# Kernel tuning notes

Hardware: AMD Instinct MI355X
Metric: run time of the kernel (lower is better)

## Reference

```python
import jax, jax.numpy as jnp
import numpy as np

B, D, O, A, H, NL = 1024, 512, 8, 64, 1024, 2

def setup_inputs() -> dict:
    key = jax.random.key(0)
    ks = jax.random.split(key, 8)
    s = 0.02
    return {
        "state": jax.random.normal(ks[0], (B, D), jnp.float32),
        # option network: Linear(D,H) -> ReLU -> Linear(H,O)
        "ow1": jax.random.normal(ks[1], (D, H), jnp.float32) * s, "ob1": jnp.zeros((H,), jnp.float32),
        "ow2": jax.random.normal(ks[2], (H, O), jnp.float32) * s, "ob2": jnp.zeros((O,), jnp.float32),
        # stacked action networks (one per option): Linear(D,H) -> act -> [Linear(H,H) -> act]*(NL-1) -> Linear(H,A)
        "aw1": jax.random.normal(ks[3], (O, D, H), jnp.float32) * s, "ab1": jnp.zeros((O, H), jnp.float32),
        "awh": jax.random.normal(ks[4], (O, NL - 1, H, H), jnp.float32) * s, "abh": jnp.zeros((O, NL - 1, H), jnp.float32),
        "awo": jax.random.normal(ks[5], (O, H, A), jnp.float32) * s, "abo": jnp.zeros((O, A), jnp.float32),
        # termination network: Linear(D,H) -> ReLU -> Linear(H,1) -> Sigmoid
        "tw1": jax.random.normal(ks[6], (D, H), jnp.float32) * s, "tb1": jnp.zeros((H,), jnp.float32),
        "tw2": jax.random.normal(ks[7], (H, 1), jnp.float32) * s, "tb2": jnp.zeros((1,), jnp.float32),
    }

def reference(state, ow1, ob1, ow2, ob2, aw1, ab1, awh, abh, awo, abo, tw1, tb1, tw2, tb2):
    # option routing: softmax over option logits, then per-sample multinomial draw
    opt_logits = jax.nn.relu(state @ ow1 + ob1) @ ow2 + ob2            # [B, O]
    option_probs = jax.nn.softmax(opt_logits, axis=-1)
    # categorical(logits) == multinomial(softmax(logits), 1); fixed key = deterministic reference
    sel = jax.random.categorical(jax.random.key(42), opt_logits, axis=-1)  # [B] int
    # run all experts batched (grouped GEMM), then gather the selected expert's q-values
    h = jax.nn.relu(jnp.einsum('bd,odh->boh', state, aw1) + ab1)       # [B, O, H]
    for i in range(awh.shape[1]):  # fixed small layer count
        h = jax.nn.relu(jnp.einsum('boh,ohg->bog', h, awh[:, i]) + abh[:, i])
    q = jnp.einsum('boh,oha->boa', h, awo) + abo                       # [B, O, A]
    q_sel = jnp.take_along_axis(q, sel[:, None, None], axis=1)[:, 0]   # [B, A]
    action_probs = jax.nn.softmax(q_sel, axis=-1)
    selected_actions = jnp.argmax(action_probs, axis=-1)               # [B]
    termination_prob = jax.nn.sigmoid(jax.nn.relu(state @ tw1 + tb1) @ tw2 + tb2)  # [B, 1]
    return option_probs, action_probs, termination_prob, jnp.argmax(option_probs, axis=-1), selected_actions
```

## Files before the change

### kernel.cpp

```cpp
#include <hip/hip_runtime.h>
#include <math.h>

#define Bsz 1024
#define Din 512
#define Hdim 1024
#define Aact 64
#define MAXT 23
#define NXCD 8

#define OFF_ACT   8192
#define OFF_TERM  73728
#define OFF_OARG  74752
#define OFF_SACT  75776

typedef __attribute__((ext_vector_type(8))) short bf16x8;
typedef __attribute__((ext_vector_type(4))) float f32x4;

__device__ __forceinline__ unsigned rotl32(unsigned x, int d){ return (x << d) | (x >> (32 - d)); }

__device__ __forceinline__ void threefry_042(unsigned& x0, unsigned& x1){
  const unsigned ks0 = 0u, ks1 = 42u, ks2 = 0x1BD11BDAu ^ 0u ^ 42u;
  x0 += ks0; x1 += ks1;
#define TFR(r) { x0 += x1; x1 = rotl32(x1, r); x1 ^= x0; }
  TFR(13) TFR(15) TFR(26) TFR(6)  x0 += ks1; x1 += ks2 + 1u;
  TFR(17) TFR(29) TFR(16) TFR(24) x0 += ks2; x1 += ks0 + 2u;
  TFR(13) TFR(15) TFR(26) TFR(6)  x0 += ks0; x1 += ks1 + 3u;
  TFR(17) TFR(29) TFR(16) TFR(24) x0 += ks1; x1 += ks2 + 4u;
  TFR(13) TFR(15) TFR(26) TFR(6)  x0 += ks2; x1 += ks0 + 5u;
#undef TFR
}

__device__ __forceinline__ float gumbel_at(int idx){
  unsigned x0 = 0u, x1 = (unsigned)idx;
  threefry_042(x0, x1);
  unsigned bits = x0 ^ x1;
  float f = __uint_as_float((bits >> 9) | 0x3F800000u) - 1.0f;
  float u = fmaxf(f, 1.1754944e-38f);
  return -logf(-logf(u));
}

__device__ __forceinline__ unsigned short bf16_rne(float x){
  unsigned u = __float_as_uint(x);
  return (unsigned short)((u + 0x7FFFu + ((u >> 16) & 1u)) >> 16);
}
__device__ __forceinline__ float bf16_tof(unsigned short h){
  return __uint_as_float(((unsigned)h) << 16);
}

__global__ __launch_bounds__(256)
void convert_state(const float* __restrict__ st, unsigned short* __restrict__ hi,
                   unsigned short* __restrict__ lo)
{
  const int i = (blockIdx.x * 256 + threadIdx.x) * 4;
  float4 v = *(const float4*)(st + i);
  ushort4 h, l;
  h.x = bf16_rne(v.x); l.x = bf16_rne(v.x - bf16_tof(h.x));
  h.y = bf16_rne(v.y); l.y = bf16_rne(v.y - bf16_tof(h.y));
  h.z = bf16_rne(v.z); l.z = bf16_rne(v.z - bf16_tof(h.z));
  h.w = bf16_rne(v.w); l.w = bf16_rne(v.w - bf16_tof(h.w));
  *(ushort4*)(hi + i) = h;
  *(ushort4*)(lo + i) = l;
}

template<bool DENSE, bool GATHER, bool HILOOUT>
__global__ __launch_bounds__(256)
void mfma_gemm(const unsigned short* __restrict__ Ahi, const unsigned short* __restrict__ Alo,
               int lda,
               const float* __restrict__ W0, const float* __restrict__ W1, long long wstride,
               const float* __restrict__ b0, const float* __restrict__ b1, int bstride,
               float* __restrict__ C0, float* __restrict__ C1,
               unsigned short* __restrict__ Chi, unsigned short* __restrict__ Clo,
               int N, int K,
               const int* __restrict__ order, const int* __restrict__ offsets,
               const int* __restrict__ tlist)
{
  const float* W; const float* bias; float* C;
  int mbase, r1, n0;
  if (DENSE){
    const int bid = (int)(blockIdx.x + 16u*blockIdx.y + 256u*blockIdx.z);
    const int wf = (bid & 7) * 64 + (bid >> 3);
    const int ny = wf & 15, mx = (wf >> 4) & 15, z = wf >> 8;
    mbase = mx * 64; r1 = Bsz; n0 = ny * 64;
    W = z ? W1 : W0; bias = z ? b1 : b0; C = z ? C1 : C0;
  } else {
    const int bid = (int)(blockIdx.x + gridDim.x * blockIdx.y);
    const int wf = (bid % NXCD) * ((MAXT * 16) / NXCD) + bid / NXCD;
    const int i = wf >> 4;
    if (i >= tlist[0]) return;
    const int o = tlist[1 + 2*i];
    mbase = tlist[2 + 2*i];
    r1 = offsets[o + 1];
    n0 = (wf & 15) * 64;
    W = W0 + (long long)o * wstride; bias = b0 + o * bstride; C = C0;
  }

  __shared__ unsigned short sAh[4096], sAl[4096], sBh[4096], sBl[4096];

  const int tid = threadIdx.x;
  const int wv = tid >> 6, lane = tid & 63;

  const int ar = tid & 63, akb = tid >> 6;
  int grow = mbase + ar;
  int arow = grow < r1 ? grow : mbase;
  if (GATHER) arow = order[arow];
  const unsigned short* pAh = Ahi + (long long)arow * lda;
  const unsigned short* pAl = Alo + (long long)arow * lda;

  const int qr = (wv >> 1) * 32, qc = (wv & 1) * 32;

  f32x4 acc[2][2];
#pragma unroll
  for (int a = 0; a < 2; a++)
#pragma unroll
    for (int b = 0; b < 2; b++) acc[a][b] = (f32x4){0.f, 0.f, 0.f, 0.f};

  for (int kt = 0; kt < K; kt += 64){
#pragma unroll
    for (int h = 0; h < 2; h++){
      const int kbl = akb + h*4;
      *(float4*)(sAh + kbl*512 + ar*8) = *(const float4*)(pAh + kt + kbl*8);
      *(float4*)(sAl + kbl*512 + ar*8) = *(const float4*)(pAl + kt + kbl*8);
    }
#pragma unroll
    for (int rp = 0; rp < 8; rp++){
      const int kl = wv * 16 + rp * 2;
      const int kbl = kl >> 3, e = kl & 7;
      const float v0 = W[(long long)(kt + kl) * N + n0 + lane];
      const float v1 = W[(long long)(kt + kl + 1) * N + n0 + lane];
      const unsigned short h0 = bf16_rne(v0), h1 = bf16_rne(v1);
      const unsigned short l0 = bf16_rne(v0 - bf16_tof(h0)), l1 = bf16_rne(v1 - bf16_tof(h1));
      *(unsigned*)(sBh + kbl*512 + lane*8 + e) = ((unsigned)h1 << 16) | h0;
      *(unsigned*)(sBl + kbl*512 + lane*8 + e) = ((unsigned)l1 << 16) | l0;
    }
    __syncthreads();
#pragma unroll
    for (int kg = 0; kg < 2; kg++){
      const int g = (kg*4 + (lane >> 4)) * 512, li = lane & 15;
      bf16x8 a0h = *(const bf16x8*)(sAh + g + (qr + li) * 8);
      bf16x8 a1h = *(const bf16x8*)(sAh + g + (qr + 16 + li) * 8);
      bf16x8 a0l = *(const bf16x8*)(sAl + g + (qr + li) * 8);
      bf16x8 a1l = *(const bf16x8*)(sAl + g + (qr + 16 + li) * 8);
      bf16x8 b0h = *(const bf16x8*)(sBh + g + (qc + li) * 8);
      bf16x8 b1h = *(const bf16x8*)(sBh + g + (qc + 16 + li) * 8);
      bf16x8 b0l = *(const bf16x8*)(sBl + g + (qc + li) * 8);
      bf16x8 b1l = *(const bf16x8*)(sBl + g + (qc + 16 + li) * 8);
      acc[0][0] = __builtin_amdgcn_mfma_f32_16x16x32_bf16(a0h, b0h, acc[0][0], 0, 0, 0);
      acc[0][1] = __builtin_amdgcn_mfma_f32_16x16x32_bf16(a0h, b1h, acc[0][1], 0, 0, 0);
      acc[1][0] = __builtin_amdgcn_mfma_f32_16x16x32_bf16(a1h, b0h, acc[1][0], 0, 0, 0);
      acc[1][1] = __builtin_amdgcn_mfma_f32_16x16x32_bf16(a1h, b1h, acc[1][1], 0, 0, 0);
      acc[0][0] = __builtin_amdgcn_mfma_f32_16x16x32_bf16(a0h, b0l, acc[0][0], 0, 0, 0);
      acc[0][1] = __builtin_amdgcn_mfma_f32_16x16x32_bf16(a0h, b1l, acc[0][1], 0, 0, 0);
      acc[1][0] = __builtin_amdgcn_mfma_f32_16x16x32_bf16(a1h, b0l, acc[1][0], 0, 0, 0);
      acc[1][1] = __builtin_amdgcn_mfma_f32_16x16x32_bf16(a1h, b1l, acc[1][1], 0, 0, 0);
      acc[0][0] = __builtin_amdgcn_mfma_f32_16x16x32_bf16(a0l, b0h, acc[0][0], 0, 0, 0);
      acc[0][1] = __builtin_amdgcn_mfma_f32_16x16x32_bf16(a0l, b1h, acc[0][1], 0, 0, 0);
      acc[1][0] = __builtin_amdgcn_mfma_f32_16x16x32_bf16(a1l, b0h, acc[1][0], 0, 0, 0);
      acc[1][1] = __builtin_amdgcn_mfma_f32_16x16x32_bf16(a1l, b1h, acc[1][1], 0, 0, 0);
    }
    __syncthreads();
  }

#pragma unroll
  for (int rb = 0; rb < 2; rb++)
#pragma unroll
    for (int cb = 0; cb < 2; cb++){
      const int col = n0 + qc + cb*16 + (lane & 15);
      const float bv = bias[col];
#pragma unroll
      for (int r = 0; r < 4; r++){
        const int row = mbase + qr + rb*16 + (lane >> 4)*4 + r;
        if (row < r1){
          const float v = fmaxf(acc[rb][cb][r] + bv, 0.f);
          if (HILOOUT){
            const unsigned short h = bf16_rne(v);
            Chi[(long long)row * N + col] = h;
            Clo[(long long)row * N + col] = bf16_rne(v - bf16_tof(h));
          } else {
            C[(long long)row * N + col] = v;
          }
        }
      }
    }
}

__global__ __launch_bounds__(256)
void q_mfma(const unsigned short* __restrict__ Ahi, const unsigned short* __restrict__ Alo,
            const float* __restrict__ awo,
            float* __restrict__ qp,
            const int* __restrict__ offsets, const int* __restrict__ tlist)
{
  const int i = blockIdx.x;
  if (i >= tlist[0]) return;
  const int o = tlist[1 + 2*i];
  const int mbase = tlist[2 + 2*i];
  const int r1 = offsets[o + 1];
  const int kb = blockIdx.y;
  const float* W = awo + (long long)o * Hdim * Aact;

  __shared__ unsigned short sAh[4096], sAl[4096], sBh[4096], sBl[4096];

  const int tid = threadIdx.x;
  const int wv = tid >> 6, lane = tid & 63;
  const int ar = tid & 63, akb = tid >> 6;
  int grow = mbase + ar;
  int arow = grow < r1 ? grow : mbase;
  const unsigned short* pAh = Ahi + (long long)arow * Hdim;
  const unsigned short* pAl = Alo + (long long)arow * Hdim;

  const int qr = (wv >> 1) * 32, qc = (wv & 1) * 32;

  f32x4 acc[2][2];
#pragma unroll
  for (int a = 0; a < 2; a++)
#pragma unroll
    for (int b = 0; b < 2; b++) acc[a][b] = (f32x4){0.f, 0.f, 0.f, 0.f};

  const int kbeg = kb * 256, kend = kbeg + 256;
  for (int kt = kbeg; kt < kend; kt += 64){
#pragma unroll
    for (int h = 0; h < 2; h++){
      const int kbl = akb + h*4;
      *(float4*)(sAh + kbl*512 + ar*8) = *(const float4*)(pAh + kt + kbl*8);
      *(float4*)(sAl + kbl*512 + ar*8) = *(const float4*)(pAl + kt + kbl*8);
    }
#pragma unroll
    for (int rp = 0; rp < 8; rp++){
      const int kl = wv * 16 + rp * 2;
      const int kbl = kl >> 3, e = kl & 7;
      const float v0 = W[(kt + kl) * Aact + lane];
      const float v1 = W[(kt + kl + 1) * Aact + lane];
      const unsigned short h0 = bf16_rne(v0), h1 = bf16_rne(v1);
      const unsigned short l0 = bf16_rne(v0 - bf16_tof(h0)), l1 = bf16_rne(v1 - bf16_tof(h1));
      *(unsigned*)(sBh + kbl*512 + lane*8 + e) = ((unsigned)h1 << 16) | h0;
      *(unsigned*)(sBl + kbl*512 + lane*8 + e) = ((unsigned)l1 << 16) | l0;
    }
    __syncthreads();
#pragma unroll
    for (int kg = 0; kg < 2; kg++){
      const int g = (kg*4 + (lane >> 4)) * 512, li = lane & 15;
      bf16x8 a0h = *(const bf16x8*)(sAh + g + (qr + li) * 8);
      bf16x8 a1h = *(const bf16x8*)(sAh + g + (qr + 16 + li) * 8);
      bf16x8 a0l = *(const bf16x8*)(sAl + g + (qr + li) * 8);
      bf16x8 a1l = *(const bf16x8*)(sAl + g + (qr + 16 + li) * 8);
      bf16x8 b0h = *(const bf16x8*)(sBh + g + (qc + li) * 8);
      bf16x8 b1h = *(const bf16x8*)(sBh + g + (qc + 16 + li) * 8);
      bf16x8 b0l = *(const bf16x8*)(sBl + g + (qc + li) * 8);
      bf16x8 b1l = *(const bf16x8*)(sBl + g + (qc + 16 + li) * 8);
      acc[0][0] = __builtin_amdgcn_mfma_f32_16x16x32_bf16(a0h, b0h, acc[0][0], 0, 0, 0);
      acc[0][1] = __builtin_amdgcn_mfma_f32_16x16x32_bf16(a0h, b1h, acc[0][1], 0, 0, 0);
      acc[1][0] = __builtin_amdgcn_mfma_f32_16x16x32_bf16(a1h, b0h, acc[1][0], 0, 0, 0);
      acc[1][1] = __builtin_amdgcn_mfma_f32_16x16x32_bf16(a1h, b1h, acc[1][1], 0, 0, 0);
      acc[0][0] = __builtin_amdgcn_mfma_f32_16x16x32_bf16(a0h, b0l, acc[0][0], 0, 0, 0);
      acc[0][1] = __builtin_amdgcn_mfma_f32_16x16x32_bf16(a0h, b1l, acc[0][1], 0, 0, 0);
      acc[1][0] = __builtin_amdgcn_mfma_f32_16x16x32_bf16(a1h, b0l, acc[1][0], 0, 0, 0);
      acc[1][1] = __builtin_amdgcn_mfma_f32_16x16x32_bf16(a1h, b1l, acc[1][1], 0, 0, 0);
      acc[0][0] = __builtin_amdgcn_mfma_f32_16x16x32_bf16(a0l, b0h, acc[0][0], 0, 0, 0);
      acc[0][1] = __builtin_amdgcn_mfma_f32_16x16x32_bf16(a0l, b1h, acc[0][1], 0, 0, 0);
      acc[1][0] = __builtin_amdgcn_mfma_f32_16x16x32_bf16(a1l, b0h, acc[1][0], 0, 0, 0);
      acc[1][1] = __builtin_amdgcn_mfma_f32_16x16x32_bf16(a1l, b1h, acc[1][1], 0, 0, 0);
    }
    __syncthreads();
  }

#pragma unroll
  for (int rb = 0; rb < 2; rb++)
#pragma unroll
    for (int cb = 0; cb < 2; cb++){
      const int col = qc + cb*16 + (lane & 15);
#pragma unroll
      for (int r = 0; r < 4; r++){
        const int row = mbase + qr + rb*16 + (lane >> 4)*4 + r;
        if (row < r1)
          qp[((long long)kb * Bsz + row) * Aact + col] = acc[rb][cb][r];
      }
    }
}

__global__ __launch_bounds__(64)
void act_kernel(const float* __restrict__ qp, const float* __restrict__ abo,
                const int* __restrict__ order, const int* __restrict__ offsets,
                float* __restrict__ out)
{
  const int r = blockIdx.x;
  int o = 0;
#pragma unroll
  for (int i = 1; i < 8; ++i) if (offsets[i] <= r) o = i;
  const int a = threadIdx.x;
  const long long idx = (long long)r * Aact + a;
  float q = qp[idx] + qp[(long long)Bsz*Aact + idx] + qp[2ll*Bsz*Aact + idx]
          + qp[3ll*Bsz*Aact + idx] + abo[o * Aact + a];
  float m = q;
#pragma unroll
  for (int off = 32; off; off >>= 1) m = fmaxf(m, __shfl_xor(m, off));
  float e = expf(q - m);
  float s = e;
#pragma unroll
  for (int off = 32; off; off >>= 1) s += __shfl_xor(s, off);
  const int b = order[r];
  out[OFF_ACT + b * Aact + a] = e / s;
  unsigned long long msk = __ballot(q == m);
  if (a == 0) out[OFF_SACT + b] = (float)__builtin_ctzll(msk);
}

__global__ __launch_bounds__(256)
void head_kernel(const float* __restrict__ h1, const float* __restrict__ th,
                 const float* __restrict__ ow2, const float* __restrict__ ob2,
                 const float* __restrict__ tw2, const float* __restrict__ tb2,
                 float* __restrict__ out, int* __restrict__ sel)
{
  const int b = blockIdx.x;
  const int t = threadIdx.x;
  const float* hrow = h1 + b * Hdim;
  const float* trow = th + b * Hdim;

  float acc[8] = {}; float accT = 0.f;
  for (int k = t; k < Hdim; k += 256){
    float hv = hrow[k];
    const float* w = ow2 + k * 8;
#pragma unroll
    for (int o2 = 0; o2 < 8; ++o2) acc[o2] += hv * w[o2];
    accT += trow[k] * tw2[k];
  }
#pragma unroll
  for (int o2 = 0; o2 < 8; ++o2)
    for (int off = 32; off; off >>= 1) acc[o2] += __shfl_down(acc[o2], off);
  for (int off = 32; off; off >>= 1) accT += __shfl_down(accT, off);

  __shared__ float wred[4][9];
  __shared__ float logits[8];
  __shared__ float gum[8];
  const int wave = t >> 6, lane = t & 63;
  if (lane == 0){
#pragma unroll
    for (int o2 = 0; o2 < 8; ++o2) wred[wave][o2] = acc[o2];
    wred[wave][8] = accT;
  }
  __syncthreads();
  if (t < 9){
    float s = wred[0][t] + wred[1][t] + wred[2][t] + wred[3][t];
    if (t < 8) logits[t] = s + ob2[t];
    else       out[OFF_TERM + b] = 1.f / (1.f + expf(-(s + tb2[0])));
  }
  __syncthreads();
  if (t < 8) gum[t] = logits[t] + gumbel_at(b * 8 + t);
  __syncthreads();
  if (t == 0){
    float m = logits[0]; int am = 0;
#pragma unroll
    for (int o2 = 1; o2 < 8; ++o2) if (logits[o2] > m){ m = logits[o2]; am = o2; }
    float p[8]; float s = 0.f;
#pragma unroll
    for (int o2 = 0; o2 < 8; ++o2){ p[o2] = expf(logits[o2] - m); s += p[o2]; }
    float inv = 1.f / s;
#pragma unroll
    for (int o2 = 0; o2 < 8; ++o2) out[b * 8 + o2] = p[o2] * inv;
    out[OFF_OARG + b] = (float)am;
    float gm = gum[0]; int gs = 0;
#pragma unroll
    for (int o2 = 1; o2 < 8; ++o2) if (gum[o2] > gm){ gm = gum[o2]; gs = o2; }
    sel[b] = gs;
  }
}

__global__ void route_kernel(const int* __restrict__ sel, int* __restrict__ order,
                             int* __restrict__ offsets, int* __restrict__ tlist)
{
  __shared__ int cnt[8];
  __shared__ int base[8];
  const int t = threadIdx.x;
  if (t < 8) cnt[t] = 0;
  __syncthreads();
  const int s = sel[t];
  atomicAdd(&cnt[s], 1);
  __syncthreads();
  if (t == 0){
    int a = 0;
    for (int o = 0; o < 8; ++o){ offsets[o] = a; base[o] = a; a += cnt[o]; }
    offsets[8] = a;
    int nt = 0;
    for (int o = 0; o < 8; ++o)
      for (int mb = offsets[o]; mb < offsets[o] + cnt[o]; mb += 64){
        tlist[1 + 2*nt] = o; tlist[2 + 2*nt] = mb; ++nt;
      }
    tlist[0] = nt;
  }
  __syncthreads();
  const int pos = atomicAdd(&base[s], 1);
  order[pos] = t;
}

extern "C" void kernel_launch(void* const* d_in, const int* in_sizes, int n_in,
                              void* d_out, int out_size, void* d_ws, size_t ws_size,
                              hipStream_t stream)
{
  (void)in_sizes; (void)n_in; (void)out_size; (void)ws_size;
  const float* state = (const float*)d_in[0];
  const float* ow1   = (const float*)d_in[1];
  const float* ob1   = (const float*)d_in[2];
  const float* ow2   = (const float*)d_in[3];
  const float* ob2   = (const float*)d_in[4];
  const float* aw1   = (const float*)d_in[5];
  const float* ab1   = (const float*)d_in[6];
  const float* awh   = (const float*)d_in[7];
  const float* abh   = (const float*)d_in[8];
  const float* awo   = (const float*)d_in[9];
  const float* abo   = (const float*)d_in[10];
  const float* tw1   = (const float*)d_in[11];
  const float* tb1   = (const float*)d_in[12];
  const float* tw2   = (const float*)d_in[13];
  const float* tb2   = (const float*)d_in[14];
  float* out = (float*)d_out;

  float* h1 = (float*)d_ws;
  float* h2 = h1 + (long long)Bsz * Hdim;
  float* qp = h2 + (long long)Bsz * Hdim;
  unsigned short* sthi = (unsigned short*)(qp + 4ll * Bsz * Aact);
  unsigned short* stlo = sthi + (long long)Bsz * Din;
  unsigned short* h1hi = stlo + (long long)Bsz * Din;
  unsigned short* h1lo = h1hi + (long long)Bsz * Hdim;
  unsigned short* h2hi = h1lo + (long long)Bsz * Hdim;
  unsigned short* h2lo = h2hi + (long long)Bsz * Hdim;
  int* sel     = (int*)(h2lo + (long long)Bsz * Hdim);
  int* order   = sel + Bsz;
  int* offsets = order + Bsz;
  int* tlist   = offsets + 9;

  convert_state<<<dim3(512), 256, 0, stream>>>(state, sthi, stlo);
  mfma_gemm<true, false, false><<<dim3(16, 16, 2), 256, 0, stream>>>(
      sthi, stlo, Din, ow1, tw1, 0, ob1, tb1, 0, h1, h2, nullptr, nullptr,
      Hdim, Din, nullptr, nullptr, nullptr);
  head_kernel<<<dim3(Bsz), 256, 0, stream>>>(h1, h2, ow2, ob2, tw2, tb2, out, sel);
  route_kernel<<<dim3(1), 1024, 0, stream>>>(sel, order, offsets, tlist);
  mfma_gemm<false, true, true><<<dim3(MAXT, 16), 256, 0, stream>>>(
      sthi, stlo, Din, aw1, nullptr, (long long)Din*Hdim, ab1, nullptr, Hdim,
      nullptr, nullptr, h1hi, h1lo, Hdim, Din, order, offsets, tlist);
  mfma_gemm<false, false, true><<<dim3(MAXT, 16), 256, 0, stream>>>(
      h1hi, h1lo, Hdim, awh, nullptr, (long long)Hdim*Hdim, abh, nullptr, Hdim,
      nullptr, nullptr, h2hi, h2lo, Hdim, Hdim, nullptr, offsets, tlist);
  q_mfma<<<dim3(MAXT, 4), 256, 0, stream>>>(h2hi, h2lo, awo, qp, offsets, tlist);
  act_kernel<<<dim3(Bsz), 64, 0, stream>>>(qp, abo, order, offsets, out);
}
```

Measured before the change: 101.7 us.

## Double-buffer LDS tiles in grouped GEMM and q-projection kernels

Both MFMA GEMM kernels now keep two LDS buffers. Each iteration stages the next K-tile, including the global load and the bf16 hi/lo split of weights, while MFMAs run on the current tile, and one barrier per iteration replaces two. This is meant to hide global load latency behind matrix compute. LDS use per block doubles to 64KB, which may cut occupancy, and the staging code inside the compute phase raises register pressure.

Result: slower. 104.8 us (+3.0%).

```diff
diff --git a/kernel.cpp b/kernel.cpp
--- a/kernel.cpp
+++ b/kernel.cpp
@@ -94,7 +94,7 @@
     W = W0 + (long long)o * wstride; bias = b0 + o * bstride; C = C0;
   }
 
-  __shared__ unsigned short sAh[4096], sAl[4096], sBh[4096], sBl[4096];
+  __shared__ unsigned short sAh[8192], sAl[8192], sBh[8192], sBl[8192];
 
   const int tid = threadIdx.x;
   const int wv = tid >> 6, lane = tid & 63;
@@ -114,51 +114,65 @@
 #pragma unroll
     for (int b = 0; b < 2; b++) acc[a][b] = (f32x4){0.f, 0.f, 0.f, 0.f};
 
+#define STAGE(bf, kt) {                                                      \
+    const int bo = (bf) * 4096;                                              \
+    _Pragma("unroll")                                                        \
+    for (int h = 0; h < 2; h++){                                             \
+      const int kbl = akb + h*4;                                             \
+      *(float4*)(sAh + bo + kbl*512 + ar*8) = *(const float4*)(pAh + (kt) + kbl*8); \
+      *(float4*)(sAl + bo + kbl*512 + ar*8) = *(const float4*)(pAl + (kt) + kbl*8); \
+    }                                                                        \
+    _Pragma("unroll")                                                        \
+    for (int rp = 0; rp < 8; rp++){                                          \
+      const int kl = wv * 16 + rp * 2;                                       \
+      const int kbl = kl >> 3, e = kl & 7;                                   \
+      const float v0 = W[(long long)((kt) + kl) * N + n0 + lane];            \
+      const float v1 = W[(long long)((kt) + kl + 1) * N + n0 + lane];        \
+      const unsigned short h0 = bf16_rne(v0), h1 = bf16_rne(v1);             \
+      const unsigned short l0 = bf16_rne(v0 - bf16_tof(h0));                 \
+      const unsigned short l1 = bf16_rne(v1 - bf16_tof(h1));                 \
+      *(unsigned*)(sBh + bo + kbl*512 + lane*8 + e) = ((unsigned)h1 << 16) | h0; \
+      *(unsigned*)(sBl + bo + kbl*512 + lane*8 + e) = ((unsigned)l1 << 16) | l0; \
+    } }
+
+#define COMPUTE(bf) {                                                        \
+    const int bo = (bf) * 4096;                                              \
+    _Pragma("unroll")                                                        \
+    for (int kg = 0; kg < 2; kg++){                                          \
+      const int g = bo + (kg*4 + (lane >> 4)) * 512, li = lane & 15;         \
+      bf16x8 a0h = *(const bf16x8*)(sAh + g + (qr + li) * 8);                \
+      bf16x8 a1h = *(const bf16x8*)(sAh + g + (qr + 16 + li) * 8);           \
+      bf16x8 a0l = *(const bf16x8*)(sAl + g + (qr + li) * 8);                \
+      bf16x8 a1l = *(const bf16x8*)(sAl + g + (qr + 16 + li) * 8);           \
+      bf16x8 b0h = *(const bf16x8*)(sBh + g + (qc + li) * 8);                \
+      bf16x8 b1h = *(const bf16x8*)(sBh + g + (qc + 16 + li) * 8);           \
+      bf16x8 b0l = *(const bf16x8*)(sBl + g + (qc + li) * 8);                \
+      bf16x8 b1l = *(const bf16x8*)(sBl + g + (qc + 16 + li) * 8);           \
+      acc[0][0] = __builtin_amdgcn_mfma_f32_16x16x32_bf16(a0h, b0h, acc[0][0], 0, 0, 0); \
+      acc[0][1] = __builtin_amdgcn_mfma_f32_16x16x32_bf16(a0h, b1h, acc[0][1], 0, 0, 0); \
+      acc[1][0] = __builtin_amdgcn_mfma_f32_16x16x32_bf16(a1h, b0h, acc[1][0], 0, 0, 0); \
+      acc[1][1] = __builtin_amdgcn_mfma_f32_16x16x32_bf16(a1h, b1h, acc[1][1], 0, 0, 0); \
+      acc[0][0] = __builtin_amdgcn_mfma_f32_16x16x32_bf16(a0h, b0l, acc[0][0], 0, 0, 0); \
+      acc[0][1] = __builtin_amdgcn_mfma_f32_16x16x32_bf16(a0h, b1l, acc[0][1], 0, 0, 0); \
+      acc[1][0] = __builtin_amdgcn_mfma_f32_16x16x32_bf16(a1h, b0l, acc[1][0], 0, 0, 0); \
+      acc[1][1] = __builtin_amdgcn_mfma_f32_16x16x32_bf16(a1h, b1l, acc[1][1], 0, 0, 0); \
+      acc[0][0] = __builtin_amdgcn_mfma_f32_16x16x32_bf16(a0l, b0h, acc[0][0], 0, 0, 0); \
+      acc[0][1] = __builtin_amdgcn_mfma_f32_16x16x32_bf16(a0l, b1h, acc[0][1], 0, 0, 0); \
+      acc[1][0] = __builtin_amdgcn_mfma_f32_16x16x32_bf16(a1l, b0h, acc[1][0], 0, 0, 0); \
+      acc[1][1] = __builtin_amdgcn_mfma_f32_16x16x32_bf16(a1l, b1h, acc[1][1], 0, 0, 0); \
+    } }
+
+  STAGE(0, 0);
+  __syncthreads();
+  int buf = 0;
   for (int kt = 0; kt < K; kt += 64){
-#pragma unroll
-    for (int h = 0; h < 2; h++){
-      const int kbl = akb + h*4;
-      *(float4*)(sAh + kbl*512 + ar*8) = *(const float4*)(pAh + kt + kbl*8);
-      *(float4*)(sAl + kbl*512 + ar*8) = *(const float4*)(pAl + kt + kbl*8);
-    }
-#pragma unroll
-    for (int rp = 0; rp < 8; rp++){
-      const int kl = wv * 16 + rp * 2;
-      const int kbl = kl >> 3, e = kl & 7;
-      const float v0 = W[(long long)(kt + kl) * N + n0 + lane];
-      const float v1 = W[(long long)(kt + kl + 1) * N + n0 + lane];
-      const unsigned short h0 = bf16_rne(v0), h1 = bf16_rne(v1);
-      const unsigned short l0 = bf16_rne(v0 - bf16_tof(h0)), l1 = bf16_rne(v1 - bf16_tof(h1));
-      *(unsigned*)(sBh + kbl*512 + lane*8 + e) = ((unsigned)h1 << 16) | h0;
-      *(unsigned*)(sBl + kbl*512 + lane*8 + e) = ((unsigned)l1 << 16) | l0;
-    }
+    if (kt + 64 < K) STAGE(buf ^ 1, kt + 64);
+    COMPUTE(buf);
     __syncthreads();
-#pragma unroll
-    for (int kg = 0; kg < 2; kg++){
-      const int g = (kg*4 + (lane >> 4)) * 512, li = lane & 15;
-      bf16x8 a0h = *(const bf16x8*)(sAh + g + (qr + li) * 8);
-      bf16x8 a1h = *(const bf16x8*)(sAh + g + (qr + 16 + li) * 8);
-      bf16x8 a0l = *(const bf16x8*)(sAl + g + (qr + li) * 8);
-      bf16x8 a1l = *(const bf16x8*)(sAl + g + (qr + 16 + li) * 8);
-      bf16x8 b0h = *(const bf16x8*)(sBh + g + (qc + li) * 8);
-      bf16x8 b1h = *(const bf16x8*)(sBh + g + (qc + 16 + li) * 8);
-      bf16x8 b0l = *(const bf16x8*)(sBl + g + (qc + li) * 8);
-      bf16x8 b1l = *(const bf16x8*)(sBl + g + (qc + 16 + li) * 8);
-      acc[0][0] = __builtin_amdgcn_mfma_f32_16x16x32_bf16(a0h, b0h, acc[0][0], 0, 0, 0);
-      acc[0][1] = __builtin_amdgcn_mfma_f32_16x16x32_bf16(a0h, b1h, acc[0][1], 0, 0, 0);
-      acc[1][0] = __builtin_amdgcn_mfma_f32_16x16x32_bf16(a1h, b0h, acc[1][0], 0, 0, 0);
-      acc[1][1] = __builtin_amdgcn_mfma_f32_16x16x32_bf16(a1h, b1h, acc[1][1], 0, 0, 0);
-      acc[0][0] = __builtin_amdgcn_mfma_f32_16x16x32_bf16(a0h, b0l, acc[0][0], 0, 0, 0);
-      acc[0][1] = __builtin_amdgcn_mfma_f32_16x16x32_bf16(a0h, b1l, acc[0][1], 0, 0, 0);
-      acc[1][0] = __builtin_amdgcn_mfma_f32_16x16x32_bf16(a1h, b0l, acc[1][0], 0, 0, 0);
-      acc[1][1] = __builtin_amdgcn_mfma_f32_16x16x32_bf16(a1h, b1l, acc[1][1], 0, 0, 0);
-      acc[0][0] = __builtin_amdgcn_mfma_f32_16x16x32_bf16(a0l, b0h, acc[0][0], 0, 0, 0);
-      acc[0][1] = __builtin_amdgcn_mfma_f32_16x16x32_bf16(a0l, b1h, acc[0][1], 0, 0, 0);
-      acc[1][0] = __builtin_amdgcn_mfma_f32_16x16x32_bf16(a1l, b0h, acc[1][0], 0, 0, 0);
-      acc[1][1] = __builtin_amdgcn_mfma_f32_16x16x32_bf16(a1l, b1h, acc[1][1], 0, 0, 0);
-    }
-    __syncthreads();
-  }
+    buf ^= 1;
+  }
+#undef STAGE
+#undef COMPUTE
 
 #pragma unroll
   for (int rb = 0; rb < 2; rb++)
@@ -197,7 +211,7 @@
   const int kb = blockIdx.y;
   const float* W = awo + (long long)o * Hdim * Aact;
 
-  __shared__ unsigned short sAh[4096], sAl[4096], sBh[4096], sBl[4096];
+  __shared__ unsigned short sAh[8192], sAl[8192], sBh[8192], sBl[8192];
 
   const int tid = threadIdx.x;
   const int wv = tid >> 6, lane = tid & 63;
@@ -215,52 +229,66 @@
 #pragma unroll
     for (int b = 0; b < 2; b++) acc[a][b] = (f32x4){0.f, 0.f, 0.f, 0.f};
 
+#define STAGE(bf, kt) {                                                      \
+    const int bo = (bf) * 4096;                                              \
+    _Pragma("unroll")                                                        \
+    for (int h = 0; h < 2; h++){                                             \
+      const int kbl = akb + h*4;                                             \
+      *(float4*)(sAh + bo + kbl*512 + ar*8) = *(const float4*)(pAh + (kt) + kbl*8); \
+      *(float4*)(sAl + bo + kbl*512 + ar*8) = *(const float4*)(pAl + (kt) + kbl*8); \
+    }                                                                        \
+    _Pragma("unroll")                                                        \
+    for (int rp = 0; rp < 8; rp++){                                          \
+      const int kl = wv * 16 + rp * 2;                                       \
+      const int kbl = kl >> 3, e = kl & 7;                                   \
+      const float v0 = W[((kt) + kl) * Aact + lane];                         \
+      const float v1 = W[((kt) + kl + 1) * Aact + lane];                     \
+      const unsigned short h0 = bf16_rne(v0), h1 = bf16_rne(v1);             \
+      const unsigned short l0 = bf16_rne(v0 - bf16_tof(h0));                 \
+      const unsigned short l1 = bf16_rne(v1 - bf16_tof(h1));                 \
+      *(unsigned*)(sBh + bo + kbl*512 + lane*8 + e) = ((unsigned)h1 << 16) | h0; \
+      *(unsigned*)(sBl + bo + kbl*512 + lane*8 + e) = ((unsigned)l1 << 16) | l0; \
+    } }
+
+#define COMPUTE(bf) {                                                        \
+    const int bo = (bf) * 4096;                                              \
+    _Pragma("unroll")                                                        \
+    for (int kg = 0; kg < 2; kg++){                                          \
+      const int g = bo + (kg*4 + (lane >> 4)) * 512, li = lane & 15;         \
+      bf16x8 a0h = *(const bf16x8*)(sAh + g + (qr + li) * 8);                \
+      bf16x8 a1h = *(const bf16x8*)(sAh + g + (qr + 16 + li) * 8);           \
+      bf16x8 a0l = *(const bf16x8*)(sAl + g + (qr + li) * 8);                \
+      bf16x8 a1l = *(const bf16x8*)(sAl + g + (qr + 16 + li) * 8);           \
+      bf16x8 b0h = *(const bf16x8*)(sBh + g + (qc + li) * 8);                \
+      bf16x8 b1h = *(const bf16x8*)(sBh + g + (qc + 16 + li) * 8);           \
+      bf16x8 b0l = *(const bf16x8*)(sBl + g + (qc + li) * 8);                \
+      bf16x8 b1l = *(const bf16x8*)(sBl + g + (qc + 16 + li) * 8);           \
+      acc[0][0] = __builtin_amdgcn_mfma_f32_16x16x32_bf16(a0h, b0h, acc[0][0], 0, 0, 0); \
+      acc[0][1] = __builtin_amdgcn_mfma_f32_16x16x32_bf16(a0h, b1h, acc[0][1], 0, 0, 0); \
+      acc[1][0] = __builtin_amdgcn_mfma_f32_16x16x32_bf16(a1h, b0h, acc[1][0], 0, 0, 0); \
+      acc[1][1] = __builtin_amdgcn_mfma_f32_16x16x32_bf16(a1h, b1h, acc[1][1], 0, 0, 0); \
+      acc[0][0] = __builtin_amdgcn_mfma_f32_16x16x32_bf16(a0h, b0l, acc[0][0], 0, 0, 0); \
+      acc[0][1] = __builtin_amdgcn_mfma_f32_16x16x32_bf16(a0h, b1l, acc[0][1], 0, 0, 0); \
+      acc[1][0] = __builtin_amdgcn_mfma_f32_16x16x32_bf16(a1h, b0l, acc[1][0], 0, 0, 0); \
+      acc[1][1] = __builtin_amdgcn_mfma_f32_16x16x32_bf16(a1h, b1l, acc[1][1], 0, 0, 0); \
+      acc[0][0] = __builtin_amdgcn_mfma_f32_16x16x32_bf16(a0l, b0h, acc[0][0], 0, 0, 0); \
+      acc[0][1] = __builtin_amdgcn_mfma_f32_16x16x32_bf16(a0l, b1h, acc[0][1], 0, 0, 0); \
+      acc[1][0] = __builtin_amdgcn_mfma_f32_16x16x32_bf16(a1l, b0h, acc[1][0], 0, 0, 0); \
+      acc[1][1] = __builtin_amdgcn_mfma_f32_16x16x32_bf16(a1l, b1h, acc[1][1], 0, 0, 0); \
+    } }
+
   const int kbeg = kb * 256, kend = kbeg + 256;
+  STAGE(0, kbeg);
+  __syncthreads();
+  int buf = 0;
   for (int kt = kbeg; kt < kend; kt += 64){
-#pragma unroll
-    for (int h = 0; h < 2; h++){
-      const int kbl = akb + h*4;
-      *(float4*)(sAh + kbl*512 + ar*8) = *(const float4*)(pAh + kt + kbl*8);
-      *(float4*)(sAl + kbl*512 + ar*8) = *(const float4*)(pAl + kt + kbl*8);
-    }
-#pragma unroll
-    for (int rp = 0; rp < 8; rp++){
-      const int kl = wv * 16 + rp * 2;
-      const int kbl = kl >> 3, e = kl & 7;
-      const float v0 = W[(kt + kl) * Aact + lane];
-      const float v1 = W[(kt + kl + 1) * Aact + lane];
-      const unsigned short h0 = bf16_rne(v0), h1 = bf16_rne(v1);
-      const unsigned short l0 = bf16_rne(v0 - bf16_tof(h0)), l1 = bf16_rne(v1 - bf16_tof(h1));
-      *(unsigned*)(sBh + kbl*512 + lane*8 + e) = ((unsigned)h1 << 16) | h0;
-      *(unsigned*)(sBl + kbl*512 + lane*8 + e) = ((unsigned)l1 << 16) | l0;
-    }
+    if (kt + 64 < kend) STAGE(buf ^ 1, kt + 64);
+    COMPUTE(buf);
     __syncthreads();
-#pragma unroll
-    for (int kg = 0; kg < 2; kg++){
-      const int g = (kg*4 + (lane >> 4)) * 512, li = lane & 15;
-      bf16x8 a0h = *(const bf16x8*)(sAh + g + (qr + li) * 8);
-      bf16x8 a1h = *(const bf16x8*)(sAh + g + (qr + 16 + li) * 8);
-      bf16x8 a0l = *(const bf16x8*)(sAl + g + (qr + li) * 8);
-      bf16x8 a1l = *(const bf16x8*)(sAl + g + (qr + 16 + li) * 8);
-      bf16x8 b0h = *(const bf16x8*)(sBh + g + (qc + li) * 8);
-      bf16x8 b1h = *(const bf16x8*)(sBh + g + (qc + 16 + li) * 8);
-      bf16x8 b0l = *(const bf16x8*)(sBl + g + (qc + li) * 8);
-      bf16x8 b1l = *(const bf16x8*)(sBl + g + (qc + 16 + li) * 8);
-      acc[0][0] = __builtin_amdgcn_mfma_f32_16x16x32_bf16(a0h, b0h, acc[0][0], 0, 0, 0);
-      acc[0][1] = __builtin_amdgcn_mfma_f32_16x16x32_bf16(a0h, b1h, acc[0][1], 0, 0, 0);
-      acc[1][0] = __builtin_amdgcn_mfma_f32_16x16x32_bf16(a1h, b0h, acc[1][0], 0, 0, 0);
-      acc[1][1] = __builtin_amdgcn_mfma_f32_16x16x32_bf16(a1h, b1h, acc[1][1], 0, 0, 0);
-      acc[0][0] = __builtin_amdgcn_mfma_f32_16x16x32_bf16(a0h, b0l, acc[0][0], 0, 0, 0);
-      acc[0][1] = __builtin_amdgcn_mfma_f32_16x16x32_bf16(a0h, b1l, acc[0][1], 0, 0, 0);
-      acc[1][0] = __builtin_amdgcn_mfma_f32_16x16x32_bf16(a1h, b0l, acc[1][0], 0, 0, 0);
-      acc[1][1] = __builtin_amdgcn_mfma_f32_16x16x32_bf16(a1h, b1l, acc[1][1], 0, 0, 0);
-      acc[0][0] = __builtin_amdgcn_mfma_f32_16x16x32_bf16(a0l, b0h, acc[0][0], 0, 0, 0);
-      acc[0][1] = __builtin_amdgcn_mfma_f32_16x16x32_bf16(a0l, b1h, acc[0][1], 0, 0, 0);
-      acc[1][0] = __builtin_amdgcn_mfma_f32_16x16x32_bf16(a1l, b0h, acc[1][0], 0, 0, 0);
-      acc[1][1] = __builtin_amdgcn_mfma_f32_16x16x32_bf16(a1l, b1h, acc[1][1], 0, 0, 0);
-    }
-    __syncthreads();
-  }
+    buf ^= 1;
+  }
+#undef STAGE
+#undef COMPUTE
 
 #pragma unroll
   for (int rb = 0; rb < 2; rb++)
```
